# Performance work log

Measured on AMD Instinct MI355X. Metric: run time of the kernel, lower is better.

Reference implementation:

```python
import jax, jax.numpy as jnp
import numpy as np

NEG_SLOPE = 0.2


def setup_inputs() -> dict:
    key = jax.random.key(0)
    k1, k2, k3 = jax.random.split(key, 3)
    bs, n_agents, input_dim = 32, 512, 128
    n_heads, hidden_dim = 8, 64
    h = jax.random.normal(k1, (bs, n_agents, input_dim), dtype=jnp.float32)
    # Linear(input_dim, n_heads*hidden_dim, bias=False), stored as [in, out]
    W = jax.random.normal(k2, (input_dim, n_heads * hidden_dim), dtype=jnp.float32) * (1.0 / np.sqrt(input_dim))
    # xavier_uniform with gain=1.414 on shape (1, n_heads, 2*hidden_dim)
    fan = n_heads + 2 * hidden_dim
    bound = 1.414 * np.sqrt(6.0 / fan)
    att_a = jax.random.uniform(k3, (1, n_heads, 2 * hidden_dim), dtype=jnp.float32,
                               minval=-bound, maxval=bound)
    return {"h": h, "W": W, "att_a": att_a}


def reference(h, W, att_a):
    bs, n_agents, _ = h.shape
    n_heads = att_a.shape[1]
    hidden_dim = att_a.shape[2] // 2
    # h_prime: [bs, n_heads, n_agents, hidden_dim]
    h_prime = (h @ W).reshape(bs, n_agents, n_heads, hidden_dim).transpose(0, 2, 1, 3)
    # Additive score decomposes exactly: (a1.h_i + a2.h_j) == sum(cat(h_i,h_j)*a)
    a_src = att_a[0, :, :hidden_dim]   # [n_heads, hidden_dim]
    a_dst = att_a[0, :, hidden_dim:]   # [n_heads, hidden_dim]
    e_src = jnp.einsum('bhnd,hd->bhn', h_prime, a_src)  # score contribution of node i (row)
    e_dst = jnp.einsum('bhnd,hd->bhn', h_prime, a_dst)  # contribution of node j (col)
    e = e_src[:, :, :, None] + e_dst[:, :, None, :]     # [bs, n_heads, n, n]
    e = jnp.where(e >= 0, e, NEG_SLOPE * e)             # leaky_relu(0.2)
    attention = jax.nn.softmax(e, axis=-1)
    h_new = jnp.einsum('bhnm,bhmd->bhnd', attention, h_prime)
    return jax.nn.elu(h_new)
```

## Files before the change

kernel.cpp:

```cpp
#include <hip/hip_runtime.h>

#define BS 32
#define NA 512
#define ID 128
#define NH 8
#define HD 64
#define NHD 512
#define NEG 0.2f
#define BPAD 136
#define VSTR 520

typedef short bf16x8 __attribute__((ext_vector_type(8)));
typedef float f32x4 __attribute__((ext_vector_type(4)));
typedef int   i32x4 __attribute__((ext_vector_type(4)));

__device__ inline unsigned f2bf_bits(float x) {
  unsigned u = __float_as_uint(x);
  return (u + 0x7FFFu + ((u >> 16) & 1u)) >> 16;
}

__device__ inline void split8(const float4& x, const float4& y,
                              bf16x8& hi, bf16x8& lo) {
  float f[8] = {x.x, x.y, x.z, x.w, y.x, y.y, y.z, y.w};
  #pragma unroll
  for (int j = 0; j < 8; ++j) {
    unsigned hb = f2bf_bits(f[j]);
    float r = f[j] - __uint_as_float(hb << 16);
    unsigned lb = f2bf_bits(r);
    hi[j] = (short)hb;
    lo[j] = (short)lb;
  }
}

__device__ inline unsigned selpair(float x0, float x1) {
  return (x0 >= 0.f ? 0xFFFFu : 0u) | (x1 >= 0.f ? 0xFFFF0000u : 0u);
}

__global__ __launch_bounds__(256, 4) void k1_mfma(
    const float* __restrict__ h, const float* __restrict__ W,
    const float* __restrict__ att, float* __restrict__ hp,
    float* __restrict__ sG, float* __restrict__ tG) {
  __shared__ unsigned short Bhi[64 * BPAD];
  __shared__ unsigned short Blo[64 * BPAD];

  int blk = blockIdx.x;
  int mt = blk >> 3;
  int n0 = (blk & 7) * 64;
  int m0 = mt * 128;
  int b = mt >> 2;
  int nbase = (mt & 3) * 128;
  int head = n0 >> 6;
  int t = threadIdx.x;
  int lane = t & 63, w = t >> 6;
  int q = lane >> 4, ml = lane & 15;

  {
    int c = t & 63, kq = t >> 6;
    const float* wsrc = W + (size_t)kq * 32 * NHD + n0 + c;
    #pragma unroll 4
    for (int kk = 0; kk < 32; ++kk) {
      int k = kq * 32 + kk;
      float x = wsrc[(size_t)kk * NHD];
      unsigned hb = f2bf_bits(x);
      float r = x - __uint_as_float(hb << 16);
      Bhi[c * BPAD + k] = (unsigned short)hb;
      Blo[c * BPAD + k] = (unsigned short)f2bf_bits(r);
    }
  }
  __syncthreads();

  f32x4 acc[2][4];
  #pragma unroll
  for (int mf = 0; mf < 2; ++mf)
    #pragma unroll
    for (int nf = 0; nf < 4; ++nf)
      acc[mf][nf] = (f32x4){0.f, 0.f, 0.f, 0.f};

  const float* A0 = h + (size_t)(m0 + w * 32 + ml) * ID;

  #pragma unroll
  for (int ks = 0; ks < 4; ++ks) {
    int ko = ks * 32 + q * 8;
    bf16x8 ah[2], al[2];
    #pragma unroll
    for (int mf = 0; mf < 2; ++mf) {
      const float* ap = A0 + mf * 16 * ID + ko;
      float4 f0 = *(const float4*)ap;
      float4 f1 = *(const float4*)(ap + 4);
      split8(f0, f1, ah[mf], al[mf]);
    }
    #pragma unroll
    for (int nf = 0; nf < 4; ++nf) {
      int bo = (nf * 16 + ml) * BPAD + ko;
      bf16x8 bh = *(const bf16x8*)&Bhi[bo];
      bf16x8 bl = *(const bf16x8*)&Blo[bo];
      #pragma unroll
      for (int mf = 0; mf < 2; ++mf) {
        acc[mf][nf] = __builtin_amdgcn_mfma_f32_16x16x32_bf16(ah[mf], bh, acc[mf][nf], 0, 0, 0);
        acc[mf][nf] = __builtin_amdgcn_mfma_f32_16x16x32_bf16(ah[mf], bl, acc[mf][nf], 0, 0, 0);
        acc[mf][nf] = __builtin_amdgcn_mfma_f32_16x16x32_bf16(al[mf], bh, acc[mf][nf], 0, 0, 0);
      }
    }
  }

  {
    float* ob = hp + (((size_t)b * NH + head) * NA + nbase + w * 32) * HD + ml;
    #pragma unroll
    for (int mf = 0; mf < 2; ++mf)
      #pragma unroll
      for (int nf = 0; nf < 4; ++nf)
        #pragma unroll
        for (int r = 0; r < 4; ++r)
          ob[(size_t)(mf * 16 + q * 4 + r) * HD + nf * 16] = acc[mf][nf][r];
  }

  {
    float a_s[4], a_d[4];
    #pragma unroll
    for (int nf = 0; nf < 4; ++nf) {
      a_s[nf] = att[head * 128 + nf * 16 + ml];
      a_d[nf] = att[head * 128 + 64 + nf * 16 + ml];
    }
    #pragma unroll
    for (int mf = 0; mf < 2; ++mf) {
      #pragma unroll
      for (int r = 0; r < 4; ++r) {
        float sp = 0.f, tp = 0.f;
        #pragma unroll
        for (int nf = 0; nf < 4; ++nf) {
          float c = acc[mf][nf][r];
          sp += c * a_s[nf]; tp += c * a_d[nf];
        }
        #pragma unroll
        for (int m = 1; m < 16; m <<= 1) {
          sp += __shfl_xor(sp, m, 64);
          tp += __shfl_xor(tp, m, 64);
        }
        if (ml == 0) {
          int row = nbase + w * 32 + mf * 16 + q * 4 + r;
          size_t o = ((size_t)b * NH + head) * NA + row;
          sG[o] = sp; tG[o] = tp;
        }
      }
    }
  }
}

__global__ __launch_bounds__(512) void k2_flash(
    const float* __restrict__ hp, const float* __restrict__ sG,
    const float* __restrict__ tG, float* __restrict__ out) {
  __shared__ unsigned short VTh[64 * VSTR];
  __shared__ unsigned short VTl[64 * VSTR];
  __shared__ uint4 wpk[256];
  __shared__ float tS[NA]; __shared__ float sS[NA];
  __shared__ float sA[NA]; __shared__ float sB[NA];
  __shared__ float red[8];

  int bh = blockIdx.x;
  int t = threadIdx.x;
  int lane = t & 63, w = t >> 6;
  int q = lane >> 4, ml = lane & 15;
  const float* vb = hp + (size_t)bh * NA * HD;

  float tj = tG[(size_t)bh * NA + t];
  float sj = sG[(size_t)bh * NA + t];
  tS[t] = tj; sS[t] = sj;
  {
    float m = tj;
    #pragma unroll
    for (int d = 32; d; d >>= 1) m = fmaxf(m, __shfl_xor(m, d, 64));
    if (lane == 0) red[w] = m;
  }
  __syncthreads();
  float tmax = fmaxf(fmaxf(fmaxf(red[0], red[1]), fmaxf(red[2], red[3])),
                     fmaxf(fmaxf(red[4], red[5]), fmaxf(red[6], red[7])));
  {
    float y = sj + tmax;
    float lr = fmaxf(y, 0.2f * y);
    sA[t] = __expf(y - lr);
    sB[t] = __expf(0.2f * y - lr);
  }
  if (t < 256) {
    float t0 = tS[2 * t], t1 = tS[2 * t + 1];
    float wp0 = __expf(t0 - tmax), wp1 = __expf(t1 - tmax);
    float wn0 = __expf(0.2f * (t0 - tmax)), wn1 = __expf(0.2f * (t1 - tmax));
    unsigned h0 = f2bf_bits(wp0), h1 = f2bf_bits(wp1);
    unsigned l0 = f2bf_bits(wp0 - __uint_as_float(h0 << 16));
    unsigned l1 = f2bf_bits(wp1 - __uint_as_float(h1 << 16));
    unsigned n0 = f2bf_bits(wn0), n1 = f2bf_bits(wn1);
    unsigned m0 = f2bf_bits(wn0 - __uint_as_float(n0 << 16));
    unsigned m1 = f2bf_bits(wn1 - __uint_as_float(n1 << 16));
    uint4 pk;
    pk.x = h0 | (h1 << 16); pk.y = l0 | (l1 << 16);
    pk.z = n0 | (n1 << 16); pk.w = m0 | (m1 << 16);
    wpk[t] = pk;
  }
  {
    int d = t & 63, jb = (t >> 6) * 2;
    #pragma unroll 4
    for (int k = 0; k < 32; ++k) {
      int j0 = jb + k * 16;
      float v0 = vb[(size_t)j0 * HD + d];
      float v1 = vb[(size_t)(j0 + 1) * HD + d];
      unsigned h0 = f2bf_bits(v0), h1 = f2bf_bits(v1);
      unsigned l0 = f2bf_bits(v0 - __uint_as_float(h0 << 16));
      unsigned l1 = f2bf_bits(v1 - __uint_as_float(h1 << 16));
      *(unsigned*)&VTh[d * VSTR + j0] = h0 | (h1 << 16);
      *(unsigned*)&VTl[d * VSTR + j0] = l0 | (l1 << 16);
    }
  }
  __syncthreads();

  int ri = w * 64;
  float sIr[4];
  #pragma unroll
  for (int mf = 0; mf < 4; ++mf) sIr[mf] = sS[ri + mf * 16 + ml];

  f32x4 acc1[4][4], acc2[4][4], aD1[4], aD2[4];
  #pragma unroll
  for (int mf = 0; mf < 4; ++mf) {
    #pragma unroll
    for (int nf = 0; nf < 4; ++nf) {
      acc1[mf][nf] = (f32x4){0.f, 0.f, 0.f, 0.f};
      acc2[mf][nf] = (f32x4){0.f, 0.f, 0.f, 0.f};
    }
    aD1[mf] = (f32x4){0.f, 0.f, 0.f, 0.f};
    aD2[mf] = (f32x4){0.f, 0.f, 0.f, 0.f};
  }

  bf16x8 ONESB;
  {
    int ov = (ml == 0) ? (int)0x3F803F80 : 0;
    i32x4 o = {ov, ov, ov, ov};
    ONESB = __builtin_bit_cast(bf16x8, o);
  }

  #pragma unroll 1
  for (int ch = 0; ch < 16; ++ch) {
    int j0q = ch * 32 + q * 8;
    float4 tqa = *(const float4*)&tS[j0q];
    float4 tqb = *(const float4*)&tS[j0q + 4];
    uint4 wk0 = wpk[(j0q >> 1) + 0];
    uint4 wk1 = wpk[(j0q >> 1) + 1];
    uint4 wk2 = wpk[(j0q >> 1) + 2];
    uint4 wk3 = wpk[(j0q >> 1) + 3];
    bf16x8 vh[4], vl[4];
    #pragma unroll
    for (int nf = 0; nf < 4; ++nf) {
      int dd = nf * 16 + ml;
      vh[nf] = *(const bf16x8*)&VTh[dd * VSTR + j0q];
      vl[nf] = *(const bf16x8*)&VTl[dd * VSTR + j0q];
    }
    #pragma unroll
    for (int mf = 0; mf < 4; ++mf) {
      float si = sIr[mf];
      unsigned s0 = selpair(si + tqa.x, si + tqa.y);
      unsigned s1 = selpair(si + tqa.z, si + tqa.w);
      unsigned s2 = selpair(si + tqb.x, si + tqb.y);
      unsigned s3 = selpair(si + tqb.z, si + tqb.w);
      i32x4 u1h = {(int)(wk0.x & s0), (int)(wk1.x & s1), (int)(wk2.x & s2), (int)(wk3.x & s3)};
      i32x4 u1l = {(int)(wk0.y & s0), (int)(wk1.y & s1), (int)(wk2.y & s2), (int)(wk3.y & s3)};
      i32x4 u2h = {(int)(wk0.z & ~s0), (int)(wk1.z & ~s1), (int)(wk2.z & ~s2), (int)(wk3.z & ~s3)};
      i32x4 u2l = {(int)(wk0.w & ~s0), (int)(wk1.w & ~s1), (int)(wk2.w & ~s2), (int)(wk3.w & ~s3)};
      bf16x8 p1h = __builtin_bit_cast(bf16x8, u1h);
      bf16x8 p1l = __builtin_bit_cast(bf16x8, u1l);
      bf16x8 p2h = __builtin_bit_cast(bf16x8, u2h);
      bf16x8 p2l = __builtin_bit_cast(bf16x8, u2l);
      #pragma unroll
      for (int nf = 0; nf < 4; ++nf) {
        acc1[mf][nf] = __builtin_amdgcn_mfma_f32_16x16x32_bf16(p1h, vh[nf], acc1[mf][nf], 0, 0, 0);
        acc1[mf][nf] = __builtin_amdgcn_mfma_f32_16x16x32_bf16(p1h, vl[nf], acc1[mf][nf], 0, 0, 0);
        acc1[mf][nf] = __builtin_amdgcn_mfma_f32_16x16x32_bf16(p1l, vh[nf], acc1[mf][nf], 0, 0, 0);
        acc2[mf][nf] = __builtin_amdgcn_mfma_f32_16x16x32_bf16(p2h, vh[nf], acc2[mf][nf], 0, 0, 0);
        acc2[mf][nf] = __builtin_amdgcn_mfma_f32_16x16x32_bf16(p2h, vl[nf], acc2[mf][nf], 0, 0, 0);
        acc2[mf][nf] = __builtin_amdgcn_mfma_f32_16x16x32_bf16(p2l, vh[nf], acc2[mf][nf], 0, 0, 0);
      }
      aD1[mf] = __builtin_amdgcn_mfma_f32_16x16x32_bf16(p1h, ONESB, aD1[mf], 0, 0, 0);
      aD1[mf] = __builtin_amdgcn_mfma_f32_16x16x32_bf16(p1l, ONESB, aD1[mf], 0, 0, 0);
      aD2[mf] = __builtin_amdgcn_mfma_f32_16x16x32_bf16(p2h, ONESB, aD2[mf], 0, 0, 0);
      aD2[mf] = __builtin_amdgcn_mfma_f32_16x16x32_bf16(p2l, ONESB, aD2[mf], 0, 0, 0);
    }
  }

  {
    float* ob = out + (size_t)bh * NA * HD;
    #pragma unroll
    for (int mf = 0; mf < 4; ++mf) {
      #pragma unroll
      for (int r = 0; r < 4; ++r) {
        float d1 = __shfl(aD1[mf][r], lane & 48, 64);
        float d2 = __shfl(aD2[mf][r], lane & 48, 64);
        int row = ri + mf * 16 + q * 4 + r;
        float A = sA[row], B = sB[row];
        float inv = 1.f / (A * d1 + B * d2);
        #pragma unroll
        for (int nf = 0; nf < 4; ++nf) {
          float x = (A * acc1[mf][nf][r] + B * acc2[mf][nf][r]) * inv;
          ob[(size_t)row * HD + nf * 16 + ml] = x > 0.f ? x : __expf(x) - 1.f;
        }
      }
    }
  }
}

extern "C" void kernel_launch(void* const* d_in, const int* in_sizes, int n_in,
                              void* d_out, int out_size, void* d_ws, size_t ws_size,
                              hipStream_t stream) {
  const float* h   = (const float*)d_in[0];
  const float* W   = (const float*)d_in[1];
  const float* att = (const float*)d_in[2];
  float* out = (float*)d_out;
  const size_t R = (size_t)BS * NH * NA;
  float* hp = (float*)d_ws;
  float* sG = hp + R * HD;
  float* tG = sG + R;

  k1_mfma <<<dim3(1024),    dim3(256), 0, stream>>>(h, W, att, hp, sG, tG);
  k2_flash<<<dim3(BS * NH), dim3(512), 0, stream>>>(hp, sG, tG, out);
}
```

Baseline: 146.0 us.

## Fold leaky-relu branches into single weighted P via rank-1 negative-branch correction

Rewrites the attention accumulation algebraically. The negative-slope term B*wn is treated as applying to every column, so it becomes a rank-1 correction (B*sum(wn), B*sum(wn*v)) computed once per block. The per-element weight becomes mask*(A*wp - B*wn) and is formed in registers, which halves the MFMA count (one accumulator set instead of two) and frees registers for a 2-waves-per-SIMD launch bound. The cost is per-element fp32 weight computation and bf16 hi/lo splitting inside the inner loop, plus an extra reduction pass over V during staging. Cancellation in A*wp - B*wn may also change numerical accuracy.

```diff
diff --git a/kernel.cpp b/kernel.cpp
--- a/kernel.cpp
+++ b/kernel.cpp
@@ -30,10 +30,6 @@
     hi[j] = (short)hb;
     lo[j] = (short)lb;
   }
-}
-
-__device__ inline unsigned selpair(float x0, float x1) {
-  return (x0 >= 0.f ? 0xFFFFu : 0u) | (x1 >= 0.f ? 0xFFFF0000u : 0u);
 }
 
 __global__ __launch_bounds__(256, 4) void k1_mfma(
@@ -146,15 +142,16 @@
   }
 }
 
-__global__ __launch_bounds__(512) void k2_flash(
+__global__ __launch_bounds__(512, 2) void k2_flash(
     const float* __restrict__ hp, const float* __restrict__ sG,
     const float* __restrict__ tG, float* __restrict__ out) {
   __shared__ unsigned short VTh[64 * VSTR];
   __shared__ unsigned short VTl[64 * VSTR];
-  __shared__ uint4 wpk[256];
   __shared__ float tS[NA]; __shared__ float sS[NA];
   __shared__ float sA[NA]; __shared__ float sB[NA];
-  __shared__ float red[8];
+  __shared__ float wpS[NA]; __shared__ float wnS[NA];
+  __shared__ float wnVp[8 * 64]; __shared__ float wnV[64];
+  __shared__ float red[8]; __shared__ float red2[8];
 
   int bh = blockIdx.x;
   int t = threadIdx.x;
@@ -174,58 +171,74 @@
   __syncthreads();
   float tmax = fmaxf(fmaxf(fmaxf(red[0], red[1]), fmaxf(red[2], red[3])),
                      fmaxf(fmaxf(red[4], red[5]), fmaxf(red[6], red[7])));
+
+  float wpj = __expf(tj - tmax);
+  float wnj = __expf(0.2f * (tj - tmax));
+  wpS[t] = wpj; wnS[t] = wnj;
   {
     float y = sj + tmax;
     float lr = fmaxf(y, 0.2f * y);
     sA[t] = __expf(y - lr);
     sB[t] = __expf(0.2f * y - lr);
   }
-  if (t < 256) {
-    float t0 = tS[2 * t], t1 = tS[2 * t + 1];
-    float wp0 = __expf(t0 - tmax), wp1 = __expf(t1 - tmax);
-    float wn0 = __expf(0.2f * (t0 - tmax)), wn1 = __expf(0.2f * (t1 - tmax));
-    unsigned h0 = f2bf_bits(wp0), h1 = f2bf_bits(wp1);
-    unsigned l0 = f2bf_bits(wp0 - __uint_as_float(h0 << 16));
-    unsigned l1 = f2bf_bits(wp1 - __uint_as_float(h1 << 16));
-    unsigned n0 = f2bf_bits(wn0), n1 = f2bf_bits(wn1);
-    unsigned m0 = f2bf_bits(wn0 - __uint_as_float(n0 << 16));
-    unsigned m1 = f2bf_bits(wn1 - __uint_as_float(n1 << 16));
-    uint4 pk;
-    pk.x = h0 | (h1 << 16); pk.y = l0 | (l1 << 16);
-    pk.z = n0 | (n1 << 16); pk.w = m0 | (m1 << 16);
-    wpk[t] = pk;
-  }
-  {
-    int d = t & 63, jb = (t >> 6) * 2;
-    #pragma unroll 4
-    for (int k = 0; k < 32; ++k) {
-      int j0 = jb + k * 16;
-      float v0 = vb[(size_t)j0 * HD + d];
-      float v1 = vb[(size_t)(j0 + 1) * HD + d];
-      unsigned h0 = f2bf_bits(v0), h1 = f2bf_bits(v1);
-      unsigned l0 = f2bf_bits(v0 - __uint_as_float(h0 << 16));
-      unsigned l1 = f2bf_bits(v1 - __uint_as_float(h1 << 16));
-      *(unsigned*)&VTh[d * VSTR + j0] = h0 | (h1 << 16);
-      *(unsigned*)&VTl[d * VSTR + j0] = l0 | (l1 << 16);
-    }
+  {
+    float ws = wnj;
+    #pragma unroll
+    for (int d = 32; d; d >>= 1) ws += __shfl_xor(ws, d, 64);
+    if (lane == 0) red2[w] = ws;
+  }
+  __syncthreads();
+  float wnSum = ((red2[0] + red2[1]) + (red2[2] + red2[3])) +
+                ((red2[4] + red2[5]) + (red2[6] + red2[7]));
+
+  {
+    int d = lane;
+    float part = 0.f;
+    #pragma unroll 1
+    for (int g = 0; g < 8; ++g) {
+      int j0 = w * 64 + g * 8;
+      unsigned hw0, hw1, hw2, hw3, lw0, lw1, lw2, lw3;
+#define TRPAIR(KP, HW, LW)                                                    \
+      { float v0 = vb[(size_t)(j0 + 2*(KP)) * HD + d];                        \
+        float v1 = vb[(size_t)(j0 + 2*(KP) + 1) * HD + d];                    \
+        part += wnS[j0 + 2*(KP)] * v0 + wnS[j0 + 2*(KP) + 1] * v1;            \
+        unsigned h0 = f2bf_bits(v0), h1 = f2bf_bits(v1);                      \
+        unsigned l0 = f2bf_bits(v0 - __uint_as_float(h0 << 16));              \
+        unsigned l1 = f2bf_bits(v1 - __uint_as_float(h1 << 16));              \
+        HW = h0 | (h1 << 16); LW = l0 | (l1 << 16); }
+      TRPAIR(0, hw0, lw0) TRPAIR(1, hw1, lw1)
+      TRPAIR(2, hw2, lw2) TRPAIR(3, hw3, lw3)
+#undef TRPAIR
+      uint4 hv = {hw0, hw1, hw2, hw3};
+      uint4 lv = {lw0, lw1, lw2, lw3};
+      *(uint4*)&VTh[d * VSTR + j0] = hv;
+      *(uint4*)&VTl[d * VSTR + j0] = lv;
+    }
+    wnVp[w * 64 + d] = part;
+  }
+  __syncthreads();
+  if (t < 64) {
+    float a = 0.f;
+    #pragma unroll
+    for (int ww = 0; ww < 8; ++ww) a += wnVp[ww * 64 + t];
+    wnV[t] = a;
   }
   __syncthreads();
 
   int ri = w * 64;
-  float sIr[4];
-  #pragma unroll
-  for (int mf = 0; mf < 4; ++mf) sIr[mf] = sS[ri + mf * 16 + ml];
-
-  f32x4 acc1[4][4], acc2[4][4], aD1[4], aD2[4];
+  float sIr[4], Ar[4], Br[4];
   #pragma unroll
   for (int mf = 0; mf < 4; ++mf) {
-    #pragma unroll
-    for (int nf = 0; nf < 4; ++nf) {
-      acc1[mf][nf] = (f32x4){0.f, 0.f, 0.f, 0.f};
-      acc2[mf][nf] = (f32x4){0.f, 0.f, 0.f, 0.f};
-    }
-    aD1[mf] = (f32x4){0.f, 0.f, 0.f, 0.f};
-    aD2[mf] = (f32x4){0.f, 0.f, 0.f, 0.f};
+    int rr = ri + mf * 16 + ml;
+    sIr[mf] = sS[rr]; Ar[mf] = sA[rr]; Br[mf] = sB[rr];
+  }
+
+  f32x4 acc[4][4], aD[4];
+  #pragma unroll
+  for (int mf = 0; mf < 4; ++mf) {
+    #pragma unroll
+    for (int nf = 0; nf < 4; ++nf) acc[mf][nf] = (f32x4){0.f, 0.f, 0.f, 0.f};
+    aD[mf] = (f32x4){0.f, 0.f, 0.f, 0.f};
   }
 
   bf16x8 ONESB;
@@ -238,12 +251,12 @@
   #pragma unroll 1
   for (int ch = 0; ch < 16; ++ch) {
     int j0q = ch * 32 + q * 8;
+    float4 wpa = *(const float4*)&wpS[j0q];
+    float4 wpb = *(const float4*)&wpS[j0q + 4];
+    float4 wna = *(const float4*)&wnS[j0q];
+    float4 wnb = *(const float4*)&wnS[j0q + 4];
     float4 tqa = *(const float4*)&tS[j0q];
     float4 tqb = *(const float4*)&tS[j0q + 4];
-    uint4 wk0 = wpk[(j0q >> 1) + 0];
-    uint4 wk1 = wpk[(j0q >> 1) + 1];
-    uint4 wk2 = wpk[(j0q >> 1) + 2];
-    uint4 wk3 = wpk[(j0q >> 1) + 3];
     bf16x8 vh[4], vl[4];
     #pragma unroll
     for (int nf = 0; nf < 4; ++nf) {
@@ -253,32 +266,40 @@
     }
     #pragma unroll
     for (int mf = 0; mf < 4; ++mf) {
-      float si = sIr[mf];
-      unsigned s0 = selpair(si + tqa.x, si + tqa.y);
-      unsigned s1 = selpair(si + tqa.z, si + tqa.w);
-      unsigned s2 = selpair(si + tqb.x, si + tqb.y);
-      unsigned s3 = selpair(si + tqb.z, si + tqb.w);
-      i32x4 u1h = {(int)(wk0.x & s0), (int)(wk1.x & s1), (int)(wk2.x & s2), (int)(wk3.x & s3)};
-      i32x4 u1l = {(int)(wk0.y & s0), (int)(wk1.y & s1), (int)(wk2.y & s2), (int)(wk3.y & s3)};
-      i32x4 u2h = {(int)(wk0.z & ~s0), (int)(wk1.z & ~s1), (int)(wk2.z & ~s2), (int)(wk3.z & ~s3)};
-      i32x4 u2l = {(int)(wk0.w & ~s0), (int)(wk1.w & ~s1), (int)(wk2.w & ~s2), (int)(wk3.w & ~s3)};
-      bf16x8 p1h = __builtin_bit_cast(bf16x8, u1h);
-      bf16x8 p1l = __builtin_bit_cast(bf16x8, u1l);
-      bf16x8 p2h = __builtin_bit_cast(bf16x8, u2h);
-      bf16x8 p2l = __builtin_bit_cast(bf16x8, u2l);
+      float si = sIr[mf], A = Ar[mf], B = Br[mf];
+      float c0 = (si + tqa.x >= 0.f) ? fmaf(A, wpa.x, -(B * wna.x)) : 0.f;
+      float c1 = (si + tqa.y >= 0.f) ? fmaf(A, wpa.y, -(B * wna.y)) : 0.f;
+      float c2 = (si + tqa.z >= 0.f) ? fmaf(A, wpa.z, -(B * wna.z)) : 0.f;
+      float c3 = (si + tqa.w >= 0.f) ? fmaf(A, wpa.w, -(B * wna.w)) : 0.f;
+      float c4 = (si + tqb.x >= 0.f) ? fmaf(A, wpb.x, -(B * wnb.x)) : 0.f;
+      float c5 = (si + tqb.y >= 0.f) ? fmaf(A, wpb.y, -(B * wnb.y)) : 0.f;
+      float c6 = (si + tqb.z >= 0.f) ? fmaf(A, wpb.z, -(B * wnb.z)) : 0.f;
+      float c7 = (si + tqb.w >= 0.f) ? fmaf(A, wpb.w, -(B * wnb.w)) : 0.f;
+      unsigned h0 = f2bf_bits(c0), h1 = f2bf_bits(c1), h2 = f2bf_bits(c2),
+               h3 = f2bf_bits(c3), h4 = f2bf_bits(c4), h5 = f2bf_bits(c5),
+               h6 = f2bf_bits(c6), h7 = f2bf_bits(c7);
+      i32x4 uh = {(int)(h0 | (h1 << 16)), (int)(h2 | (h3 << 16)),
+                  (int)(h4 | (h5 << 16)), (int)(h6 | (h7 << 16))};
+      unsigned l0 = f2bf_bits(c0 - __uint_as_float(h0 << 16));
+      unsigned l1 = f2bf_bits(c1 - __uint_as_float(h1 << 16));
+      unsigned l2 = f2bf_bits(c2 - __uint_as_float(h2 << 16));
+      unsigned l3 = f2bf_bits(c3 - __uint_as_float(h3 << 16));
+      unsigned l4 = f2bf_bits(c4 - __uint_as_float(h4 << 16));
+      unsigned l5 = f2bf_bits(c5 - __uint_as_float(h5 << 16));
+      unsigned l6 = f2bf_bits(c6 - __uint_as_float(h6 << 16));
+      unsigned l7 = f2bf_bits(c7 - __uint_as_float(h7 << 16));
+      i32x4 ul = {(int)(l0 | (l1 << 16)), (int)(l2 | (l3 << 16)),
+                  (int)(l4 | (l5 << 16)), (int)(l6 | (l7 << 16))};
+      bf16x8 Ph = __builtin_bit_cast(bf16x8, uh);
+      bf16x8 Pl = __builtin_bit_cast(bf16x8, ul);
       #pragma unroll
       for (int nf = 0; nf < 4; ++nf) {
-        acc1[mf][nf] = __builtin_amdgcn_mfma_f32_16x16x32_bf16(p1h, vh[nf], acc1[mf][nf], 0, 0, 0);
-        acc1[mf][nf] = __builtin_amdgcn_mfma_f32_16x16x32_bf16(p1h, vl[nf], acc1[mf][nf], 0, 0, 0);
-        acc1[mf][nf] = __builtin_amdgcn_mfma_f32_16x16x32_bf16(p1l, vh[nf], acc1[mf][nf], 0, 0, 0);
-        acc2[mf][nf] = __builtin_amdgcn_mfma_f32_16x16x32_bf16(p2h, vh[nf], acc2[mf][nf], 0, 0, 0);
-        acc2[mf][nf] = __builtin_amdgcn_mfma_f32_16x16x32_bf16(p2h, vl[nf], acc2[mf][nf], 0, 0, 0);
-        acc2[mf][nf] = __builtin_amdgcn_mfma_f32_16x16x32_bf16(p2l, vh[nf], acc2[mf][nf], 0, 0, 0);
+        acc[mf][nf] = __builtin_amdgcn_mfma_f32_16x16x32_bf16(Ph, vh[nf], acc[mf][nf], 0, 0, 0);
+        acc[mf][nf] = __builtin_amdgcn_mfma_f32_16x16x32_bf16(Pl, vh[nf], acc[mf][nf], 0, 0, 0);
+        acc[mf][nf] = __builtin_amdgcn_mfma_f32_16x16x32_bf16(Ph, vl[nf], acc[mf][nf], 0, 0, 0);
       }
-      aD1[mf] = __builtin_amdgcn_mfma_f32_16x16x32_bf16(p1h, ONESB, aD1[mf], 0, 0, 0);
-      aD1[mf] = __builtin_amdgcn_mfma_f32_16x16x32_bf16(p1l, ONESB, aD1[mf], 0, 0, 0);
-      aD2[mf] = __builtin_amdgcn_mfma_f32_16x16x32_bf16(p2h, ONESB, aD2[mf], 0, 0, 0);
-      aD2[mf] = __builtin_amdgcn_mfma_f32_16x16x32_bf16(p2l, ONESB, aD2[mf], 0, 0, 0);
+      aD[mf] = __builtin_amdgcn_mfma_f32_16x16x32_bf16(Ph, ONESB, aD[mf], 0, 0, 0);
+      aD[mf] = __builtin_amdgcn_mfma_f32_16x16x32_bf16(Pl, ONESB, aD[mf], 0, 0, 0);
     }
   }
 
@@ -288,15 +309,15 @@
     for (int mf = 0; mf < 4; ++mf) {
       #pragma unroll
       for (int r = 0; r < 4; ++r) {
-        float d1 = __shfl(aD1[mf][r], lane & 48, 64);
-        float d2 = __shfl(aD2[mf][r], lane & 48, 64);
+        float dv = __shfl(aD[mf][r], lane & 48, 64);
         int row = ri + mf * 16 + q * 4 + r;
-        float A = sA[row], B = sB[row];
-        float inv = 1.f / (A * d1 + B * d2);
+        float Brow = sB[row];
+        float inv = 1.f / fmaf(Brow, wnSum, dv);
         #pragma unroll
         for (int nf = 0; nf < 4; ++nf) {
-          float x = (A * acc1[mf][nf][r] + B * acc2[mf][nf][r]) * inv;
-          ob[(size_t)row * HD + nf * 16 + ml] = x > 0.f ? x : __expf(x) - 1.f;
+          int d = nf * 16 + ml;
+          float x = fmaf(Brow, wnV[d], acc[mf][nf][r]) * inv;
+          ob[(size_t)row * HD + d] = x > 0.f ? x : __expf(x) - 1.f;
         }
       }
     }
```

Result: faster. 132.3 us (-9.4%).
